# Performance work log

Measured on AMD Instinct MI355X. Metric: run time of the kernel, lower is better.

Reference implementation:

```python
import jax, jax.numpy as jnp
import numpy as np

B, N, C = 256, 100000, 511          # batch, memory slots, concept dim
D = C + 1                            # retrieved feature dim (deltas channel + memory row)
KEY_SIZE = 64
TOTAL = 2 * KEY_SIZE + D             # qkv_size * num_heads (num_heads = 1)


def setup_inputs() -> dict:
    key = jax.random.key(0)
    ks = jax.random.split(key, 8)
    s = 0.02
    return {
        "c": jax.random.normal(ks[0], (B, C), jnp.float32),
        "mem_c": jax.random.normal(ks[1], (N, C), jnp.float32),
        "Wqkv": jax.random.normal(ks[2], (D, TOTAL), jnp.float32) * s,
        "bqkv": jnp.zeros((TOTAL,), jnp.float32),
        "g_qkv": jnp.ones((TOTAL,), jnp.float32),
        "b_qkv": jnp.zeros((TOTAL,), jnp.float32),
        "g_mem": jnp.ones((D,), jnp.float32),
        "b_mem": jnp.zeros((D,), jnp.float32),
        "W1": jax.random.normal(ks[3], (D, D), jnp.float32) * s,
        "b1": jnp.zeros((D,), jnp.float32),
        "W2": jax.random.normal(ks[4], (D, D), jnp.float32) * s,
        "b2": jnp.zeros((D,), jnp.float32),
        "Ws1": jax.random.normal(ks[5], (D, D), jnp.float32) * s,
        "bs1": jnp.zeros((D,), jnp.float32),
        "Ws2": jax.random.normal(ks[6], (D, C), jnp.float32) * s,
        "bs2": jnp.zeros((C,), jnp.float32),
        "k": 64,
    }


def _layer_norm(x, g, b, eps=1e-5):
    mu = jnp.mean(x, axis=-1, keepdims=True)
    var = jnp.var(x, axis=-1, keepdims=True)
    return (x - mu) * jax.lax.rsqrt(var + eps) * g + b


def reference(c, mem_c, Wqkv, bqkv, g_qkv, b_qkv, g_mem, b_mem,
              W1, b1, W2, b2, Ws1, bs1, Ws2, bs2, k):
    # ----- _query: delta = dot-product similarity, topk, gather -----
    tau = c @ mem_c.T                                   # [B, N]
    deltas, idx = jax.lax.top_k(tau, k)                 # [B, k]
    gathered = mem_c[idx]                               # [B, k, C]
    mems = jnp.concatenate([deltas[..., None], gathered], axis=-1)  # [B, k, D]

    d = mems.shape[-1]
    key_size = (Wqkv.shape[1] - d) // 2

    # ----- _mhdpa: qkv projection + LN + single-head attention -----
    qkv = _layer_norm(mems @ Wqkv + bqkv, g_qkv, b_qkv)  # [B, k, 2*key+D]
    q = qkv[..., :key_size] * (key_size ** -0.5)
    kk = qkv[..., key_size:2 * key_size]
    v = qkv[..., 2 * key_size:]
    scores = jnp.einsum('bik,bjk->bij', q, kk)           # [B, k, k]
    w = jax.nn.softmax(scores, axis=-1)
    attended = jnp.einsum('bij,bjd->bid', w, v)          # [B, k, D]

    # ----- _attend_over_memory: residual LN + shared-weight MLP blocks -----
    def mlp(x):
        return jax.nn.relu(x @ W1 + b1) @ W2 + b2

    mem = _layer_norm(mems + attended, g_mem, b_mem)
    mem = _layer_norm(mlp(mem) + mem, g_mem, b_mem)
    mem = _layer_norm(mlp(mem) + mem, g_mem, b_mem)

    # ----- skip_mlp projects back to c_size -----
    c_prime = jax.nn.relu(mem @ Ws1 + bs1) @ Ws2 + bs2   # [B, k, C]
    return c_prime
```

## Files before the change

kernel.cpp:

```cpp
#include <hip/hip_runtime.h>
#include <math.h>

constexpr int BATCH = 256;
constexpr int NMEM  = 100000;
constexpr int CDIM  = 511;
constexpr int DDIM  = 512;
constexpr int TOT   = 640;
constexpr int KTOP  = 64;

__global__ __launch_bounds__(256) void tau_gemm(const float* __restrict__ cc,
                                                const float* __restrict__ memc,
                                                float* __restrict__ tau) {
    __shared__ float As[16][64];
    __shared__ float Bs[16][64];
    int bt = blockIdx.x & 3;
    int nt = blockIdx.x >> 2;
    int b0 = bt * 64, n0 = nt * 64;
    int t  = threadIdx.x;
    int ti = t & 15, tj = t >> 4;

    float acc[4][4];
#pragma unroll
    for (int i = 0; i < 4; i++)
#pragma unroll
        for (int j = 0; j < 4; j++) acc[i][j] = 0.f;

    for (int k0 = 0; k0 < CDIM; k0 += 16) {
#pragma unroll
        for (int r = 0; r < 4; r++) {
            int idx = t + r * 256;
            int row = idx >> 4, kk = idx & 15;
            int k = k0 + kk;
            As[kk][row] = (k < CDIM) ? cc[(size_t)(b0 + row) * CDIM + k] : 0.f;
            int n = n0 + row;
            Bs[kk][row] = (k < CDIM && n < NMEM) ? memc[(size_t)n * CDIM + k] : 0.f;
        }
        __syncthreads();
#pragma unroll
        for (int kk = 0; kk < 16; kk++) {
            float av[4], bv[4];
            *(float4*)av = *(const float4*)&As[kk][ti * 4];
            *(float4*)bv = *(const float4*)&Bs[kk][tj * 4];
#pragma unroll
            for (int i = 0; i < 4; i++)
#pragma unroll
                for (int j = 0; j < 4; j++)
                    acc[i][j] = fmaf(av[i], bv[j], acc[i][j]);
        }
        __syncthreads();
    }
#pragma unroll
    for (int i = 0; i < 4; i++) {
        int rowb = b0 + ti * 4 + i;
#pragma unroll
        for (int j = 0; j < 4; j++) {
            int n = n0 + tj * 4 + j;
            if (n < NMEM) tau[(size_t)rowb * NMEM + n] = acc[i][j];
        }
    }
}

constexpr int CAND_CAP = 2048;
constexpr int NBINS    = 4096;

__device__ inline unsigned mono_map(float f) {
    unsigned u = __float_as_uint(f);
    return u ^ ((u >> 31) ? 0xFFFFFFFFu : 0x80000000u);
}

__global__ __launch_bounds__(256) void topk_gather(const float* __restrict__ tau,
                                                   const float* __restrict__ memc,
                                                   float* __restrict__ mems) {
    int row = blockIdx.x;
    const float* tr = tau + (size_t)row * NMEM;
    __shared__ int   hist[NBINS];
    __shared__ int   segsum[256];
    __shared__ int   cnt;
    __shared__ int   cut_s;
    __shared__ float cv[CAND_CAP];
    __shared__ int   ci[CAND_CAP];
    __shared__ int   sel[KTOP];
    int t = threadIdx.x;

    for (int i = t; i < NBINS; i += 256) hist[i] = 0;
    if (t == 0) cnt = 0;
    __syncthreads();

    for (int n = t; n < NMEM; n += 256)
        atomicAdd(&hist[mono_map(tr[n]) >> 20], 1);
    __syncthreads();

    {
        int s = 0, base = t * 16;
#pragma unroll
        for (int i = 0; i < 16; i++) s += hist[base + i];
        segsum[t] = s;
    }
    __syncthreads();
    if (t == 0) {
        int acc = 0, cut = 0;
        for (int s = 255; s >= 0; s--) {
            if (acc + segsum[s] >= KTOP) {
                int base = s * 16;
                for (int bb = 15; bb >= 0; bb--) {
                    acc += hist[base + bb];
                    if (acc >= KTOP) { cut = base + bb; break; }
                }
                break;
            }
            acc += segsum[s];
        }
        cut_s = cut;
    }
    __syncthreads();
    unsigned cut = (unsigned)cut_s;
    for (int n = t; n < NMEM; n += 256) {
        float v = tr[n];
        if ((mono_map(v) >> 20) >= cut) {
            int p = atomicAdd(&cnt, 1);
            if (p < CAND_CAP) { cv[p] = v; ci[p] = n; }
        }
    }
    __syncthreads();
    int m = cnt < CAND_CAP ? cnt : CAND_CAP;

    if (t < 64) {
        for (int j = 0; j < KTOP; j++) {
            float bv = -INFINITY;
            int   bi = 0x7FFFFFFF, bp = -1;
            for (int p = t; p < m; p += 64) {
                float v = cv[p]; int ii = ci[p];
                if (v > bv || (v == bv && ii < bi)) { bv = v; bi = ii; bp = p; }
            }
            float wv = bv; int wi = bi;
#pragma unroll
            for (int o = 1; o < 64; o <<= 1) {
                float ov = __shfl_xor(wv, o, 64);
                int   oi = __shfl_xor(wi, o, 64);
                if (ov > wv || (ov == wv && oi < wi)) { wv = ov; wi = oi; }
            }
            if (t == 0) {
                sel[j] = wi;
                mems[((size_t)row * KTOP + j) * DDIM] = wv;
            }
            if (bp >= 0 && bi == wi) cv[bp] = -INFINITY;
        }
    }
    __syncthreads();
    for (int j = 0; j < KTOP; j++) {
        int src = sel[j];
        for (int col = t; col < CDIM; col += 256)
            mems[((size_t)row * KTOP + j) * DDIM + 1 + col] = memc[(size_t)src * CDIM + col];
    }
}

__global__ __launch_bounds__(256) void gemm_rows16(const float* __restrict__ X,
                                                   const float* __restrict__ W,
                                                   const float* __restrict__ bias,
                                                   float* __restrict__ Y,
                                                   int No, int do_relu) {
    int bx = blockIdx.x;
    int b  = bx >> 2;
    int r0 = (bx & 3) * 16;
    const float* Xb = X + ((size_t)b * 64 + r0) * DDIM;
    float*       Yb = Y + ((size_t)b * 64 + r0) * (size_t)No;
    int t = threadIdx.x;

    for (int c0 = t; c0 < No; c0 += 256) {
        float acc[16];
#pragma unroll
        for (int i = 0; i < 16; i++) acc[i] = 0.f;
        const float* Wc = W + c0;
        for (int k = 0; k < DDIM; k += 4) {
            float w0 = Wc[(size_t)(k + 0) * No];
            float w1 = Wc[(size_t)(k + 1) * No];
            float w2 = Wc[(size_t)(k + 2) * No];
            float w3 = Wc[(size_t)(k + 3) * No];
#pragma unroll
            for (int i = 0; i < 16; i++) {
                float4 x4 = *(const float4*)(Xb + i * DDIM + k);
                acc[i] = fmaf(x4.w, w3, fmaf(x4.z, w2, fmaf(x4.y, w1, fmaf(x4.x, w0, acc[i]))));
            }
        }
        float bb = bias[c0];
#pragma unroll
        for (int i = 0; i < 16; i++) {
            float v = acc[i] + bb;
            if (do_relu) v = fmaxf(v, 0.f);
            Yb[(size_t)i * No + c0] = v;
        }
    }
}

__global__ __launch_bounds__(256) void attn(const float* __restrict__ qkv,
                                            float* __restrict__ att) {
    __shared__ float smem[64 * 65 * 2];
    __shared__ float wsm[64][64];
    float (*qs)[65]  = (float(*)[65])smem;
    float (*ks)[65]  = (float(*)[65])(smem + 64 * 65);
    float (*vs)[128] = (float(*)[128])smem;

    int b = blockIdx.x, t = threadIdx.x;
    const float* Qb = qkv + (size_t)b * 64 * TOT;

    for (int idx = t; idx < 64 * 64; idx += 256) {
        int i = idx >> 6, d = idx & 63;
        qs[i][d] = Qb[(size_t)i * TOT + d];
        ks[i][d] = Qb[(size_t)i * TOT + 64 + d];
    }
    __syncthreads();
    {
        int i  = t >> 2;
        int jb = (t & 3) * 16;
#pragma unroll
        for (int jj = 0; jj < 16; jj++) {
            int j = jb + jj;
            float s = 0.f;
#pragma unroll 8
            for (int d = 0; d < 64; d++) s = fmaf(qs[i][d], ks[j][d], s);
            wsm[i][j] = s * 0.125f;
        }
    }
    __syncthreads();
    if (t < 64) {
        float mx = -INFINITY;
        for (int j = 0; j < 64; j++) mx = fmaxf(mx, wsm[t][j]);
        float sum = 0.f;
        for (int j = 0; j < 64; j++) { float e = expf(wsm[t][j] - mx); wsm[t][j] = e; sum += e; }
        float inv = 1.f / sum;
        for (int j = 0; j < 64; j++) wsm[t][j] *= inv;
    }
    __syncthreads();
    for (int ch = 0; ch < 4; ch++) {
        for (int idx = t; idx < 64 * 128; idx += 256) {
            int j = idx >> 7, d = idx & 127;
            vs[j][d] = Qb[(size_t)j * TOT + 128 + ch * 128 + d];
        }
        __syncthreads();
        int d  = t & 127;
        int i0 = (t >> 7) * 32;
        for (int i = i0; i < i0 + 32; i++) {
            float s = 0.f;
#pragma unroll 8
            for (int j = 0; j < 64; j++) s = fmaf(wsm[i][j], vs[j][d], s);
            att[((size_t)b * 64 + i) * DDIM + ch * 128 + d] = s;
        }
        __syncthreads();
    }
}

__global__ __launch_bounds__(256) void res_ln(const float* __restrict__ X,
                                              const float* __restrict__ Res,
                                              const float* __restrict__ g,
                                              const float* __restrict__ bta,
                                              float* __restrict__ Y,
                                              int width, int nrows) {
    int wave = threadIdx.x >> 6;
    int lane = threadIdx.x & 63;
    int row  = blockIdx.x * 4 + wave;
    if (row >= nrows) return;
    const float* xr = X + (size_t)row * width;
    const float* rr = Res ? Res + (size_t)row * width : nullptr;
    float vals[12];
    int per = width >> 6;
    float sum = 0.f, ssq = 0.f;
    for (int e = 0; e < per; e++) {
        int col = lane + e * 64;
        float v = xr[col];
        if (rr) v += rr[col];
        vals[e] = v; sum += v; ssq = fmaf(v, v, ssq);
    }
    for (int o = 32; o > 0; o >>= 1) {
        sum += __shfl_down(sum, o, 64);
        ssq += __shfl_down(ssq, o, 64);
    }
    sum = __shfl(sum, 0, 64);
    ssq = __shfl(ssq, 0, 64);
    float mu  = sum / width;
    float var = ssq / width - mu * mu;
    float rs  = rsqrtf(var + 1e-5f);
    float* yr = Y + (size_t)row * width;
    for (int e = 0; e < per; e++) {
        int col = lane + e * 64;
        yr[col] = (vals[e] - mu) * rs * g[col] + bta[col];
    }
}

extern "C" void kernel_launch(void* const* d_in, const int* in_sizes, int n_in,
                              void* d_out, int out_size, void* d_ws, size_t ws_size,
                              hipStream_t stream) {
    const float* cc    = (const float*)d_in[0];
    const float* memc  = (const float*)d_in[1];
    const float* Wqkv  = (const float*)d_in[2];
    const float* bqkv  = (const float*)d_in[3];
    const float* g_qkv = (const float*)d_in[4];
    const float* b_qkv = (const float*)d_in[5];
    const float* g_mem = (const float*)d_in[6];
    const float* b_mem = (const float*)d_in[7];
    const float* W1    = (const float*)d_in[8];
    const float* b1    = (const float*)d_in[9];
    const float* W2    = (const float*)d_in[10];
    const float* b2    = (const float*)d_in[11];
    const float* Ws1   = (const float*)d_in[12];
    const float* bs1   = (const float*)d_in[13];
    const float* Ws2   = (const float*)d_in[14];
    const float* bs2   = (const float*)d_in[15];
    float* out = (float*)d_out;

    float* ws   = (float*)d_ws;
    float* tau  = ws;
    float* qkv  = ws;
    float* h    = ws + 10485760;
    float* mems = ws + 25600000;
    float* Ab   = ws + 33988608;
    float* Bb   = mems;

    constexpr int NT      = (NMEM + 63) / 64;
    constexpr int NROWS   = BATCH * KTOP;
    constexpr int LN_GRID = NROWS / 4;

    tau_gemm<<<NT * 4, 256, 0, stream>>>(cc, memc, tau);
    topk_gather<<<BATCH, 256, 0, stream>>>(tau, memc, mems);

    gemm_rows16<<<BATCH * 4, 256, 0, stream>>>(mems, Wqkv, bqkv, qkv, TOT, 0);
    res_ln<<<LN_GRID, 256, 0, stream>>>(qkv, nullptr, g_qkv, b_qkv, qkv, TOT, NROWS);

    attn<<<BATCH, 256, 0, stream>>>(qkv, Ab);

    res_ln<<<LN_GRID, 256, 0, stream>>>(Ab, mems, g_mem, b_mem, Ab, DDIM, NROWS);

    gemm_rows16<<<BATCH * 4, 256, 0, stream>>>(Ab, W1, b1, h, DDIM, 1);
    gemm_rows16<<<BATCH * 4, 256, 0, stream>>>(h, W2, b2, Bb, DDIM, 0);
    res_ln<<<LN_GRID, 256, 0, stream>>>(Bb, Ab, g_mem, b_mem, Bb, DDIM, NROWS);

    gemm_rows16<<<BATCH * 4, 256, 0, stream>>>(Bb, W1, b1, h, DDIM, 1);
    gemm_rows16<<<BATCH * 4, 256, 0, stream>>>(h, W2, b2, Ab, DDIM, 0);
    res_ln<<<LN_GRID, 256, 0, stream>>>(Ab, Bb, g_mem, b_mem, Ab, DDIM, NROWS);

    gemm_rows16<<<BATCH * 4, 256, 0, stream>>>(Ab, Ws1, bs1, h, DDIM, 1);
    gemm_rows16<<<BATCH * 4, 256, 0, stream>>>(h, Ws2, bs2, out, CDIM, 0);
}
```

Before: 2.968 ms.

## Compute similarity GEMM in bf16 MFMA and rescore top-k candidates in fp32

Converts mem_c and c to zero-padded bf16 and computes the 256x100000 similarity matrix with bf16 MFMA instructions, using async global-to-LDS loads and a swizzled LDS layout, storing tau as bf16. Top-k filtering builds its histogram on bf16 keys with a widened cutoff (one extra bin and a larger candidate cap), then recomputes exact fp32 dot products for the candidates before final selection. This cuts the FLOP cost of the scalar fp32 GEMM and halves tau traffic. The risks are candidates lost to bf16 error near the cutoff, or overflow of the candidate buffer.

```diff
diff --git a/kernel.cpp b/kernel.cpp
--- a/kernel.cpp
+++ b/kernel.cpp
@@ -7,72 +7,124 @@
 constexpr int DDIM  = 512;
 constexpr int TOT   = 640;
 constexpr int KTOP  = 64;
-
-__global__ __launch_bounds__(256) void tau_gemm(const float* __restrict__ cc,
-                                                const float* __restrict__ memc,
-                                                float* __restrict__ tau) {
-    __shared__ float As[16][64];
-    __shared__ float Bs[16][64];
-    int bt = blockIdx.x & 3;
-    int nt = blockIdx.x >> 2;
-    int b0 = bt * 64, n0 = nt * 64;
-    int t  = threadIdx.x;
-    int ti = t & 15, tj = t >> 4;
-
-    float acc[4][4];
+constexpr int KPAD  = 512;
+
+typedef __attribute__((ext_vector_type(8))) short short8;
+typedef __attribute__((ext_vector_type(4))) float floatx4;
+
+__device__ __forceinline__ unsigned short rtn_bf16(float x) {
+    unsigned u = __float_as_uint(x);
+    u += 0x7FFFu + ((u >> 16) & 1);
+    return (unsigned short)(u >> 16);
+}
+
+__device__ __forceinline__ void async_ld16(void* lds, const void* g) {
+    __builtin_amdgcn_global_load_lds(
+        (const __attribute__((address_space(1))) void*)g,
+        (__attribute__((address_space(3))) void*)lds, 16, 0, 0);
+}
+
+__global__ __launch_bounds__(256) void cvt_bf16_pad(const float* __restrict__ src,
+                                                    unsigned short* __restrict__ dst,
+                                                    int nrows) {
+    size_t total = (size_t)nrows * KPAD;
+    for (size_t idx = (size_t)blockIdx.x * 256 + threadIdx.x; idx < total;
+         idx += (size_t)gridDim.x * 256) {
+        int   k = (int)(idx & (KPAD - 1));
+        size_t n = idx >> 9;
+        float v = (k < CDIM) ? src[n * CDIM + k] : 0.f;
+        dst[idx] = rtn_bf16(v);
+    }
+}
+
+__global__ __launch_bounds__(256) void tau_gemm_bf16(const unsigned short* __restrict__ A2,
+                                                     const unsigned short* __restrict__ B2,
+                                                     unsigned short* __restrict__ tau16) {
+    __shared__ unsigned short As[128 * 64];
+    __shared__ unsigned short Bs[128 * 64];
+    int bx = blockIdx.x;
+    int mt = bx & 1, nt = bx >> 1;
+    int m0 = mt * 128, n0 = nt * 128;
+    int t = threadIdx.x;
+    int wave = t >> 6, lane = t & 63;
+    int rh = wave >> 1, chf = wave & 1;
+    int l15 = lane & 15, quad = lane >> 4;
+
+    floatx4 acc[4][4];
+    floatx4 zero = {0.f, 0.f, 0.f, 0.f};
 #pragma unroll
     for (int i = 0; i < 4; i++)
 #pragma unroll
-        for (int j = 0; j < 4; j++) acc[i][j] = 0.f;
-
-    for (int k0 = 0; k0 < CDIM; k0 += 16) {
-#pragma unroll
-        for (int r = 0; r < 4; r++) {
-            int idx = t + r * 256;
-            int row = idx >> 4, kk = idx & 15;
-            int k = k0 + kk;
-            As[kk][row] = (k < CDIM) ? cc[(size_t)(b0 + row) * CDIM + k] : 0.f;
-            int n = n0 + row;
-            Bs[kk][row] = (k < CDIM && n < NMEM) ? memc[(size_t)n * CDIM + k] : 0.f;
-        }
+        for (int j = 0; j < 4; j++) acc[i][j] = zero;
+
+    int srow = t >> 3;
+    int skg  = (t & 7) ^ (srow & 7);
+
+    for (int c = 0; c < 8; c++) {
+        int k0 = c * 64;
         __syncthreads();
 #pragma unroll
-        for (int kk = 0; kk < 16; kk++) {
-            float av[4], bv[4];
-            *(float4*)av = *(const float4*)&As[kk][ti * 4];
-            *(float4*)bv = *(const float4*)&Bs[kk][tj * 4];
-#pragma unroll
-            for (int i = 0; i < 4; i++)
-#pragma unroll
-                for (int j = 0; j < 4; j++)
-                    acc[i][j] = fmaf(av[i], bv[j], acc[i][j]);
+        for (int i = 0; i < 4; i++) {
+            int rowA = i * 32 + srow;
+            const unsigned short* ga = A2 + (size_t)(m0 + rowA) * KPAD + k0 + skg * 8;
+            async_ld16((void*)(As + i * 2048 + wave * 512), (const void*)ga);
+            int rowB = n0 + i * 32 + srow;
+            if (rowB > NMEM - 1) rowB = NMEM - 1;
+            const unsigned short* gb = B2 + (size_t)rowB * KPAD + k0 + skg * 8;
+            async_ld16((void*)(Bs + i * 2048 + wave * 512), (const void*)gb);
         }
         __syncthreads();
-    }
-#pragma unroll
-    for (int i = 0; i < 4; i++) {
-        int rowb = b0 + ti * 4 + i;
-#pragma unroll
-        for (int j = 0; j < 4; j++) {
-            int n = n0 + tj * 4 + j;
-            if (n < NMEM) tau[(size_t)rowb * NMEM + n] = acc[i][j];
-        }
-    }
-}
-
-constexpr int CAND_CAP = 2048;
+#pragma unroll
+        for (int s = 0; s < 2; s++) {
+            int g = s * 4 + quad;
+            short8 af[4], bf[4];
+#pragma unroll
+            for (int mi = 0; mi < 4; mi++) {
+                int row = rh * 64 + mi * 16 + l15;
+                af[mi] = *(const short8*)&As[row * 64 + ((g ^ (row & 7)) << 3)];
+            }
+#pragma unroll
+            for (int ni = 0; ni < 4; ni++) {
+                int col = chf * 64 + ni * 16 + l15;
+                bf[ni] = *(const short8*)&Bs[col * 64 + ((g ^ (col & 7)) << 3)];
+            }
+#pragma unroll
+            for (int mi = 0; mi < 4; mi++)
+#pragma unroll
+                for (int ni = 0; ni < 4; ni++)
+                    acc[mi][ni] = __builtin_amdgcn_mfma_f32_16x16x32_bf16(
+                        af[mi], bf[ni], acc[mi][ni], 0, 0, 0);
+        }
+    }
+#pragma unroll
+    for (int mi = 0; mi < 4; mi++) {
+#pragma unroll
+        for (int ni = 0; ni < 4; ni++) {
+            int n = n0 + chf * 64 + ni * 16 + l15;
+            if (n < NMEM) {
+#pragma unroll
+                for (int r = 0; r < 4; r++) {
+                    int m = m0 + rh * 64 + mi * 16 + quad * 4 + r;
+                    tau16[(size_t)m * NMEM + n] = rtn_bf16(acc[mi][ni][r]);
+                }
+            }
+        }
+    }
+}
+
+constexpr int CAND_CAP = 4096;
 constexpr int NBINS    = 4096;
 
-__device__ inline unsigned mono_map(float f) {
-    unsigned u = __float_as_uint(f);
-    return u ^ ((u >> 31) ? 0xFFFFFFFFu : 0x80000000u);
-}
-
-__global__ __launch_bounds__(256) void topk_gather(const float* __restrict__ tau,
+__device__ __forceinline__ unsigned mono16(unsigned x) {
+    return (x ^ ((x & 0x8000u) ? 0xFFFFu : 0x8000u)) & 0xFFFFu;
+}
+
+__global__ __launch_bounds__(256) void topk_gather(const unsigned short* __restrict__ tau16,
+                                                   const float* __restrict__ cc,
                                                    const float* __restrict__ memc,
                                                    float* __restrict__ mems) {
     int row = blockIdx.x;
-    const float* tr = tau + (size_t)row * NMEM;
+    const unsigned* tr32 = (const unsigned*)(tau16 + (size_t)row * NMEM);
     __shared__ int   hist[NBINS];
     __shared__ int   segsum[256];
     __shared__ int   cnt;
@@ -86,8 +138,11 @@
     if (t == 0) cnt = 0;
     __syncthreads();
 
-    for (int n = t; n < NMEM; n += 256)
-        atomicAdd(&hist[mono_map(tr[n]) >> 20], 1);
+    for (int i = t; i < NMEM / 2; i += 256) {
+        unsigned u = tr32[i];
+        atomicAdd(&hist[mono16(u & 0xFFFFu) >> 4], 1);
+        atomicAdd(&hist[mono16(u >> 16) >> 4], 1);
+    }
     __syncthreads();
 
     {
@@ -110,19 +165,35 @@
             }
             acc += segsum[s];
         }
-        cut_s = cut;
+        cut_s = (cut > 0) ? cut - 1 : 0;
     }
     __syncthreads();
     unsigned cut = (unsigned)cut_s;
-    for (int n = t; n < NMEM; n += 256) {
-        float v = tr[n];
-        if ((mono_map(v) >> 20) >= cut) {
+    for (int i = t; i < NMEM / 2; i += 256) {
+        unsigned u = tr32[i];
+        if ((mono16(u & 0xFFFFu) >> 4) >= cut) {
             int p = atomicAdd(&cnt, 1);
-            if (p < CAND_CAP) { cv[p] = v; ci[p] = n; }
+            if (p < CAND_CAP) ci[p] = 2 * i;
+        }
+        if ((mono16(u >> 16) >> 4) >= cut) {
+            int p = atomicAdd(&cnt, 1);
+            if (p < CAND_CAP) ci[p] = 2 * i + 1;
         }
     }
     __syncthreads();
     int m = cnt < CAND_CAP ? cnt : CAND_CAP;
+
+    {
+        const float* cr = cc + (size_t)row * CDIM;
+        for (int p = t; p < m; p += 256) {
+            const float* mr = memc + (size_t)ci[p] * CDIM;
+            float s = 0.f;
+#pragma unroll 4
+            for (int k = 0; k < CDIM; k++) s = fmaf(cr[k], mr[k], s);
+            cv[p] = s;
+        }
+    }
+    __syncthreads();
 
     if (t < 64) {
         for (int j = 0; j < KTOP; j++) {
@@ -307,20 +378,24 @@
     const float* bs2   = (const float*)d_in[15];
     float* out = (float*)d_out;
 
-    float* ws   = (float*)d_ws;
-    float* tau  = ws;
-    float* qkv  = ws;
-    float* h    = ws + 10485760;
-    float* mems = ws + 25600000;
-    float* Ab   = ws + 33988608;
+    float* ws = (float*)d_ws;
+    unsigned short* B2    = (unsigned short*)ws;
+    unsigned short* tau16 = (unsigned short*)(ws + 25600000);
+    unsigned short* A2    = (unsigned short*)(ws + 38400000);
+    float* mems = ws;
+    float* qkv  = ws + 8388608;
+    float* h    = ws + 18874368;
+    float* Ab   = ws + 27262976;
     float* Bb   = mems;
 
-    constexpr int NT      = (NMEM + 63) / 64;
     constexpr int NROWS   = BATCH * KTOP;
     constexpr int LN_GRID = NROWS / 4;
-
-    tau_gemm<<<NT * 4, 256, 0, stream>>>(cc, memc, tau);
-    topk_gather<<<BATCH, 256, 0, stream>>>(tau, memc, mems);
+    constexpr int NTILES  = (NMEM + 127) / 128;
+
+    cvt_bf16_pad<<<2048, 256, 0, stream>>>(memc, B2, NMEM);
+    cvt_bf16_pad<<<64, 256, 0, stream>>>(cc, A2, BATCH);
+    tau_gemm_bf16<<<NTILES * 2, 256, 0, stream>>>(A2, B2, tau16);
+    topk_gather<<<BATCH, 256, 0, stream>>>(tau16, cc, memc, mems);
 
     gemm_rows16<<<BATCH * 4, 256, 0, stream>>>(mems, Wqkv, bqkv, qkv, TOT, 0);
     res_ln<<<LN_GRID, 256, 0, stream>>>(qkv, nullptr, g_qkv, b_qkv, qkv, TOT, NROWS);
```

After: 2.484 ms. 1.19x faster.
